# Optimization experiments

Hardware: AMD Instinct MI355X
Metric: run time of the kernel (lower is better)

The kernel has to match this reference:

```python
import jax, jax.numpy as jnp
import numpy as np

E = 8          # num_global_experts
K = 2          # top-k
D = 1024       # model_dim
H = 4096       # hidden_size_per_expert
CAP_FACTOR = 1.0


def setup_inputs() -> dict:
    key = jax.random.key(0)
    ks = jax.random.split(key, 5)
    x = jax.random.normal(ks[0], (4, 2048, D), jnp.float32)
    gate_w = jax.random.normal(ks[1], (E, D), jnp.float32) * 0.02
    fc1_w = jax.random.normal(ks[2], (E, H, D), jnp.float32) * 0.02
    fc1_b = jnp.zeros((E, 1, H), jnp.float32)
    fc2_w = jax.random.normal(ks[3], (E, H, D), jnp.float32) * 0.02
    fc2_b = jnp.zeros((E, 1, D), jnp.float32)
    return {"x": x, "gate_w": gate_w, "fc1_w": fc1_w, "fc1_b": fc1_b,
            "fc2_w": fc2_w, "fc2_b": fc2_b}


def reference(x, gate_w, fc1_w, fc1_b, fc2_w, fc2_b):
    B, S, Dm = x.shape
    xf = x.reshape(-1, Dm)                       # [N, D] tokens
    N = xf.shape[0]
    cap = int(K * CAP_FACTOR * ((N + E - 1) // E))  # expert capacity

    # ---- gating (top-k softmax, normalized) ----
    logits = xf @ gate_w.T                       # [N, E]
    scores = jax.nn.softmax(logits, axis=-1)
    topv, topi = jax.lax.top_k(scores, K)        # [N, K]
    gates = topv / jnp.sum(topv, axis=-1, keepdims=True)

    # ---- per-slot locations within each expert (sequential over K slots) ----
    offset = jnp.zeros((E,), jnp.int32)
    locs = []
    for j in range(K):
        mask = jax.nn.one_hot(topi[:, j], E, dtype=jnp.int32)   # [N, E]
        loc_in = jnp.cumsum(mask, axis=0) - 1 + offset[None, :]
        locs.append(jnp.take_along_axis(loc_in, topi[:, j:j + 1], axis=1)[:, 0])
        offset = offset + mask.sum(axis=0)
    loc = jnp.stack(locs, axis=1)                # [N, K]
    valid = loc < cap                            # capacity-dropped tokens
    flat_idx = jnp.where(valid, topi * cap + loc, 0)   # [N, K]
    w = valid.astype(xf.dtype)

    # ---- dispatch (scatter tokens into [E, cap, D], postscore => unweighted) ----
    disp = jnp.zeros((E * cap, Dm), xf.dtype)
    disp = disp.at[flat_idx.reshape(-1)].add(
        (xf[:, None, :] * w[:, :, None]).reshape(-1, Dm))
    de = disp.reshape(E, cap, Dm)

    # ---- batched expert FFN: relu(x @ fc1^T + b1) @ fc2 + b2 ----
    h = jax.nn.relu(jnp.einsum('ecd,ehd->ech', de, fc1_w) + fc1_b)
    eo = jnp.einsum('ech,ehd->ecd', h, fc2_w) + fc2_b

    # ---- combine (gather + gate-weighted sum over K slots) ----
    gathered = eo.reshape(E * cap, Dm)[flat_idx]       # [N, K, D]
    out = jnp.sum(gathered * (gates * w)[:, :, None], axis=1)
    return out.reshape(B, S, Dm)
```

## Files before the change

### kernel.cpp

```cpp
#include <hip/hip_runtime.h>
#include <hip/hip_bf16.h>
#include <stdint.h>

#define NEXP 8
#define DM   1024
#define HID  4096
#define NTOK 8192
#define CAPS 2048

#define BM 256
#define BN 256
#define BK 64

typedef __attribute__((ext_vector_type(8))) short bh8_t;
typedef __attribute__((ext_vector_type(4))) float f32x4_t;
typedef unsigned short u16;

static __device__ __forceinline__ u16 f2bf(float f) {
    __hip_bfloat16 h = __float2bfloat16(f);
    return __builtin_bit_cast(u16, h);
}
static __device__ __forceinline__ float bf2f(u16 u) {
    unsigned int x = ((unsigned int)u) << 16;
    return __builtin_bit_cast(float, x);
}

#define FENCE asm volatile("" ::: "memory")
#define BAR   do { FENCE; __builtin_amdgcn_s_barrier(); FENCE; } while (0)
#define LGKM0 do { asm volatile("s_waitcnt lgkmcnt(0)" ::: "memory"); \
                   __builtin_amdgcn_sched_barrier(0); } while (0)
#define MFMA(d, a, b) d = __builtin_amdgcn_mfma_f32_16x16x32_bf16(a, b, d, 0, 0, 0)

__global__ __launch_bounds__(256) void k_conv_bf16(const float* __restrict__ in,
                                                   u16* __restrict__ out, long n) {
    long i = ((long)blockIdx.x * 256 + threadIdx.x) * 4;
    if (i >= n) return;
    float4 v = *(const float4*)(in + i);
    ushort4 o;
    o.x = f2bf(v.x); o.y = f2bf(v.y); o.z = f2bf(v.z); o.w = f2bf(v.w);
    *(ushort4*)(out + i) = o;
}

__global__ __launch_bounds__(256) void k_transpose_w2(const float* __restrict__ in,
                                                      u16* __restrict__ out) {
    int e = blockIdx.z;
    const float* I = in + (long)e * HID * DM;
    u16* O = out + (long)e * DM * HID;
    __shared__ float t[32][33];
    int x = threadIdx.x & 31, y = threadIdx.x >> 5;
    int h0 = blockIdx.x * 32, d0 = blockIdx.y * 32;
    #pragma unroll
    for (int i = 0; i < 4; ++i)
        t[y + 8*i][x] = I[(long)(h0 + y + 8*i) * DM + d0 + x];
    __syncthreads();
    #pragma unroll
    for (int i = 0; i < 4; ++i)
        O[(long)(d0 + y + 8*i) * HID + h0 + x] = f2bf(t[x][y + 8*i]);
}

__global__ __launch_bounds__(256) void k_gating(const float* __restrict__ x,
        const float* __restrict__ gw, int* __restrict__ topi, float* __restrict__ gates) {
    __shared__ float sg[NEXP][DM];
    int tid = threadIdx.x;
    for (int i = tid; i < NEXP*DM; i += 256) ((float*)sg)[i] = gw[i];
    __syncthreads();
    int lane = tid & 63, w = tid >> 6;
    long n = (long)blockIdx.x * 4 + w;
    const float* xr = x + n * DM;
    float acc[NEXP] = {};
    for (int i = 0; i < DM/64; ++i) {
        float xv = xr[lane + i*64];
        #pragma unroll
        for (int e = 0; e < NEXP; ++e) acc[e] += xv * sg[e][lane + i*64];
    }
    #pragma unroll
    for (int e = 0; e < NEXP; ++e)
        #pragma unroll
        for (int off = 32; off; off >>= 1) acc[e] += __shfl_xor(acc[e], off);
    if (lane == 0) {
        float mx = acc[0];
        #pragma unroll
        for (int e = 1; e < NEXP; ++e) mx = fmaxf(mx, acc[e]);
        float p[NEXP];
        #pragma unroll
        for (int e = 0; e < NEXP; ++e) p[e] = expf(acc[e] - mx);
        float v0 = p[0]; int i0 = 0;
        #pragma unroll
        for (int e = 1; e < NEXP; ++e) if (p[e] > v0) { v0 = p[e]; i0 = e; }
        float v1 = -1.f; int i1 = 0;
        #pragma unroll
        for (int e = 0; e < NEXP; ++e) if (e != i0 && p[e] > v1) { v1 = p[e]; i1 = e; }
        float tot = v0 + v1;
        topi[n*2]   = i0; topi[n*2+1] = i1;
        gates[n*2]  = v0 / tot; gates[n*2+1] = v1 / tot;
    }
}

__global__ __launch_bounds__(64) void k_locate(const int* __restrict__ topi,
                                               int* __restrict__ flat) {
    int lane = threadIdx.x;
    const int TPL = NTOK / 64;
    int base = lane * TPL;
    int offset[NEXP];
    #pragma unroll
    for (int e = 0; e < NEXP; ++e) offset[e] = 0;
    for (int j = 0; j < 2; ++j) {
        unsigned long long pk = 0;
        for (int t = 0; t < TPL; ++t) {
            int e = topi[(long)(base + t)*2 + j];
            pk += 1ull << (8*e);
        }
        int cnt[NEXP], excl[NEXP];
        #pragma unroll
        for (int e = 0; e < NEXP; ++e) cnt[e] = (int)((pk >> (8*e)) & 0xff);
        #pragma unroll
        for (int e = 0; e < NEXP; ++e) {
            int v = cnt[e];
            for (int d = 1; d < 64; d <<= 1) {
                int o = __shfl_up(v, d);
                if (lane >= d) v += o;
            }
            excl[e] = v - cnt[e] + offset[e];
            offset[e] += __shfl(v, 63);
        }
        unsigned long long lo = 0, hi = 0;
        #pragma unroll
        for (int e = 0; e < 4; ++e)    lo |= (unsigned long long)(excl[e] & 0xffff) << (16*e);
        #pragma unroll
        for (int e = 4; e < NEXP; ++e) hi |= (unsigned long long)(excl[e] & 0xffff) << (16*(e-4));
        for (int t = 0; t < TPL; ++t) {
            long n = base + t;
            int e = topi[n*2 + j];
            int sh = 16 * (e & 3);
            int loc;
            if (e < 4) { loc = (int)((lo >> sh) & 0xffff); lo += 1ull << sh; }
            else       { loc = (int)((hi >> sh) & 0xffff); hi += 1ull << sh; }
            flat[n*2 + j] = (loc < CAPS) ? (e * CAPS + loc) : -1;
        }
    }
}

__global__ __launch_bounds__(256) void k_dispatch(const float* __restrict__ x,
        const int* __restrict__ flat, u16* __restrict__ disp) {
    long n = blockIdx.x;
    int tid = threadIdx.x;
    float4 v = *(const float4*)(x + n*DM + tid*4);
    ushort4 o; o.x = f2bf(v.x); o.y = f2bf(v.y); o.z = f2bf(v.z); o.w = f2bf(v.w);
    int f0 = flat[n*2], f1 = flat[n*2+1];
    if (f0 >= 0) *(ushort4*)(disp + (long)f0*DM + tid*4) = o;
    if (f1 >= 0) *(ushort4*)(disp + (long)f1*DM + tid*4) = o;
}

static __device__ __forceinline__ void stage_half(const u16* __restrict__ g, int ld,
                                                  u16* R, int wid, int lane) {
    int rlo = wid*8 + (lane >> 3);
    int cbe = ((lane & 7) ^ ((lane >> 3) & 7)) * 8;
    const u16* s0 = g + (long)rlo * ld + cbe;
    const u16* s1 = g + (long)(rlo + 64) * ld + cbe;
    u16* d0 = R + wid*512 + lane*8;
    u16* d1 = R + 4096 + wid*512 + lane*8;
    __builtin_amdgcn_global_load_lds((const __attribute__((address_space(1))) void*)s0,
        (__attribute__((address_space(3))) void*)d0, 16, 0, 0);
    __builtin_amdgcn_global_load_lds((const __attribute__((address_space(1))) void*)s1,
        (__attribute__((address_space(3))) void*)d1, 16, 0, 0);
}

template<int RELU>
__global__ __launch_bounds__(512, 2)
void k_gemm8(const u16* __restrict__ A, const u16* __restrict__ B,
             const float* __restrict__ bias, u16* __restrict__ C,
             int N, int K, long strA, long strB, long strBias, long strC)
{
    __shared__ u16 sm[2][2][2][8192];

    int gx = gridDim.x, gy = gridDim.y;
    int nwg = gx * gy * (int)gridDim.z;
    int lin = blockIdx.x + gx * (blockIdx.y + gy * blockIdx.z);
    int qq  = nwg >> 3;
    int swz = (lin & 7) * qq + (lin >> 3);
    int gxy = gx * gy;
    int bz = swz / gxy, rm = swz % gxy, by = rm / gx, bx = rm % gx;

    const u16* Ae = A + (long)bz * strA;
    const u16* Be = B + (long)bz * strB;
    const float* bi = bias + (long)bz * strBias;
    u16* Ce = C + (long)bz * strC;

    long tm = (long)by * BM, tn = (long)bx * BN;
    const u16* Abase = Ae + tm * (long)K;
    const u16* Bbase = Be + tn * (long)K;

    int tid = threadIdx.x, lane = tid & 63, wid = tid >> 6;
    int wr = wid >> 2, wc = wid & 3;

    int frow = lane & 15;
    int fc0 = (((lane >> 4) * 16)      ^ ((lane & 7) << 4)) >> 1;
    int fc1 = ((64 + (lane >> 4) * 16) ^ ((lane & 7) << 4)) >> 1;

    const int NT = K / BK;

    f32x4_t acc[8][4] = {};

    auto STG = [&](int buf, int ab, int half, int kt) {
        const u16* g = (ab ? Bbase : Abase) + (long)(half * 128) * K + (long)kt * BK;
        stage_half(g, K, &sm[buf][ab][half][0], wid, lane);
    };
    auto LDA = [&](int c, int mi, int kk) -> bh8_t {
        const u16* p = &sm[c][0][wr][0] + (mi * 16 + frow) * 64 + (kk ? fc1 : fc0);
        return *(const bh8_t*)p;
    };
    auto LDB = [&](int c, int ni, int kk) -> bh8_t {
        const u16* p = &sm[c][1][wc >> 1][0] + ((wc & 1) * 64 + ni * 16 + frow) * 64 + (kk ? fc1 : fc0);
        return *(const bh8_t*)p;
    };

    auto ktile = [&](int c, int kt, int s12, int s34, int vm) {
        bh8_t a0[4][2], a1[4][2], bf[4][2];
        #pragma unroll
        for (int mi = 0; mi < 4; ++mi) { a0[mi][0] = LDA(c, mi, 0); a0[mi][1] = LDA(c, mi, 1); }
        #pragma unroll
        for (int ni = 0; ni < 2; ++ni) { bf[ni][0] = LDB(c, ni, 0); bf[ni][1] = LDB(c, ni, 1); }
        if (s12) STG(c ^ 1, 0, 1, kt + 1);
        BAR; LGKM0;
        __builtin_amdgcn_s_setprio(1);
        #pragma unroll
        for (int mi = 0; mi < 4; ++mi)
            #pragma unroll
            for (int ni = 0; ni < 2; ++ni)
                #pragma unroll
                for (int kk = 0; kk < 2; ++kk) MFMA(acc[mi][ni], a0[mi][kk], bf[ni][kk]);
        __builtin_amdgcn_s_setprio(0);
        __builtin_amdgcn_sched_barrier(0);
        BAR;
        #pragma unroll
        for (int ni = 2; ni < 4; ++ni) { bf[ni][0] = LDB(c, ni, 0); bf[ni][1] = LDB(c, ni, 1); }
        if (s12) STG(c ^ 1, 1, 1, kt + 1);
        BAR; LGKM0;
        __builtin_amdgcn_s_setprio(1);
        #pragma unroll
        for (int mi = 0; mi < 4; ++mi)
            #pragma unroll
            for (int ni = 2; ni < 4; ++ni)
                #pragma unroll
                for (int kk = 0; kk < 2; ++kk) MFMA(acc[mi][ni], a0[mi][kk], bf[ni][kk]);
        __builtin_amdgcn_s_setprio(0);
        __builtin_amdgcn_sched_barrier(0);
        BAR;
        #pragma unroll
        for (int mi = 0; mi < 4; ++mi) { a1[mi][0] = LDA(c, mi + 4, 0); a1[mi][1] = LDA(c, mi + 4, 1); }
        if (s34) STG(c, 1, 0, kt + 2);
        BAR; LGKM0;
        __builtin_amdgcn_s_setprio(1);
        #pragma unroll
        for (int mi = 0; mi < 4; ++mi)
            #pragma unroll
            for (int ni = 0; ni < 2; ++ni)
                #pragma unroll
                for (int kk = 0; kk < 2; ++kk) MFMA(acc[mi + 4][ni], a1[mi][kk], bf[ni][kk]);
        __builtin_amdgcn_s_setprio(0);
        __builtin_amdgcn_sched_barrier(0);
        BAR;
        if (s34) STG(c, 0, 0, kt + 2);
        if (vm == 4)      { asm volatile("s_waitcnt vmcnt(4)" ::: "memory"); }
        else if (vm == 0) { asm volatile("s_waitcnt vmcnt(0)" ::: "memory"); }
        BAR; LGKM0;
        __builtin_amdgcn_s_setprio(1);
        #pragma unroll
        for (int mi = 0; mi < 4; ++mi)
            #pragma unroll
            for (int ni = 2; ni < 4; ++ni)
                #pragma unroll
                for (int kk = 0; kk < 2; ++kk) MFMA(acc[mi + 4][ni], a1[mi][kk], bf[ni][kk]);
        __builtin_amdgcn_s_setprio(0);
        __builtin_amdgcn_sched_barrier(0);
        BAR;
    };

    STG(0, 0, 0, 0); STG(0, 0, 1, 0); STG(0, 1, 0, 0); STG(0, 1, 1, 0);
    STG(1, 1, 0, 1); STG(1, 0, 0, 1);
    asm volatile("s_waitcnt vmcnt(4)" ::: "memory");
    BAR;

    int kt = 0;
    for (; kt < NT - 2; ++kt) ktile(kt & 1, kt, 1, 1, 4);
    ktile(kt & 1, kt, 1, 0, 0); ++kt;
    ktile(kt & 1, kt, 0, 0, -1);

    u16* wb = &sm[0][0][0][0] + wid * 8192;
    #pragma unroll
    for (int mi = 0; mi < 8; ++mi)
        #pragma unroll
        for (int ni = 0; ni < 4; ++ni) {
            float bv = bi[tn + wc * 64 + ni * 16 + (lane & 15)];
            #pragma unroll
            for (int r = 0; r < 4; ++r) {
                int row = mi * 16 + (lane >> 4) * 4 + r;
                int ce  = ni * 16 + (lane & 15);
                float v = acc[mi][ni][r] + bv;
                if (RELU) v = fmaxf(v, 0.f);
                wb[row * 64 + (ce ^ ((row & 7) << 3))] = f2bf(v);
            }
        }
    __syncthreads();
    long crow = tm + wr * 128;
    long ccol = tn + wc * 64 + (lane & 7) * 8;
    #pragma unroll
    for (int i = 0; i < 16; ++i) {
        int rr = i * 8 + (lane >> 3);
        bh8_t v = *(const bh8_t*)(wb + rr * 64 + (((lane & 7) * 8) ^ ((rr & 7) << 3)));
        *(bh8_t*)(Ce + (crow + rr) * N + ccol) = v;
    }
}

__global__ __launch_bounds__(256) void k_combine(const u16* __restrict__ eo,
        const int* __restrict__ flat, const float* __restrict__ gates,
        float* __restrict__ out) {
    long n = blockIdx.x;
    int tid = threadIdx.x;
    int f0 = flat[n*2], f1 = flat[n*2+1];
    float g0 = (f0 >= 0) ? gates[n*2]   : 0.f;
    float g1 = (f1 >= 0) ? gates[n*2+1] : 0.f;
    const u16* r0 = eo + (long)(f0 >= 0 ? f0 : 0) * DM;
    const u16* r1 = eo + (long)(f1 >= 0 ? f1 : 0) * DM;
    ushort4 a = *(const ushort4*)(r0 + tid*4);
    ushort4 b = *(const ushort4*)(r1 + tid*4);
    float4 o;
    o.x = g0*bf2f(a.x) + g1*bf2f(b.x);
    o.y = g0*bf2f(a.y) + g1*bf2f(b.y);
    o.z = g0*bf2f(a.z) + g1*bf2f(b.z);
    o.w = g0*bf2f(a.w) + g1*bf2f(b.w);
    *(float4*)(out + n*DM + tid*4) = o;
}

extern "C" void kernel_launch(void* const* d_in, const int* in_sizes, int n_in,
                              void* d_out, int out_size, void* d_ws, size_t ws_size,
                              hipStream_t stream) {
    const float* x    = (const float*)d_in[0];
    const float* gw   = (const float*)d_in[1];
    const float* fc1w = (const float*)d_in[2];
    const float* fc1b = (const float*)d_in[3];
    const float* fc2w = (const float*)d_in[4];
    const float* fc2b = (const float*)d_in[5];
    float* out = (float*)d_out;
    char* ws = (char*)d_ws;

    u16* disp = (u16*)(ws);
    u16* eo   = disp;
    u16* h    = (u16*)(ws + 33554432L);
    u16* w1b  = (u16*)(ws + 33554432L + 134217728L);
    u16* w2t  = (u16*)(ws + 33554432L + 134217728L + 67108864L);
    char* tail = ws + 33554432L + 134217728L + 67108864L + 67108864L;
    int*   topi  = (int*)tail;
    float* gates = (float*)(tail + 65536);
    int*   flat  = (int*)(tail + 131072);

    long n1 = (long)NEXP * HID * DM;

    hipMemsetAsync(disp, 0, (size_t)NEXP * CAPS * DM * 2, stream);
    k_conv_bf16<<<dim3(n1/1024), 256, 0, stream>>>(fc1w, w1b, n1);
    k_transpose_w2<<<dim3(HID/32, DM/32, NEXP), 256, 0, stream>>>(fc2w, w2t);
    k_gating<<<dim3(NTOK/4), 256, 0, stream>>>(x, gw, topi, gates);
    k_locate<<<dim3(1), 64, 0, stream>>>(topi, flat);
    k_dispatch<<<dim3(NTOK), 256, 0, stream>>>(x, flat, disp);
    k_gemm8<1><<<dim3(HID/BN, CAPS/BM, NEXP), 512, 0, stream>>>(
        disp, w1b, fc1b, h, HID, DM,
        (long)CAPS*DM, (long)HID*DM, (long)HID, (long)CAPS*HID);
    k_gemm8<0><<<dim3(DM/BN, CAPS/BM, NEXP), 512, 0, stream>>>(
        h, w2t, fc2b, eo, DM, HID,
        (long)CAPS*HID, (long)DM*HID, (long)DM, (long)CAPS*DM);
    k_combine<<<dim3(NTOK), 256, 0, stream>>>(eo, flat, gates, out);
}
```

Before: 471.9 us.

## Drop dispatch memset, vectorize W2 transpose, parallelize locate, relax GEMM LDS waits

Removes the zero-fill of the dispatch buffer. Unfilled capacity rows are computed independently and never gathered by combine, so the result does not depend on them. The fc2 transpose moves to 64x64 tiles with float4 loads and 16-byte bf16 stores. The single-wave locate kernel becomes a 256-thread block that stages topi in LDS and combines per-wave scans through shared sums. The GEMM also drops the explicit lgkmcnt(0) waits before each MFMA group and leaves LDS dependency waits to the compiler, which cuts stalls but adds scheduling risk.

```diff
diff --git a/kernel.cpp b/kernel.cpp
--- a/kernel.cpp
+++ b/kernel.cpp
@@ -27,8 +27,7 @@
 
 #define FENCE asm volatile("" ::: "memory")
 #define BAR   do { FENCE; __builtin_amdgcn_s_barrier(); FENCE; } while (0)
-#define LGKM0 do { asm volatile("s_waitcnt lgkmcnt(0)" ::: "memory"); \
-                   __builtin_amdgcn_sched_barrier(0); } while (0)
+#define SB0   __builtin_amdgcn_sched_barrier(0)
 #define MFMA(d, a, b) d = __builtin_amdgcn_mfma_f32_16x16x32_bf16(a, b, d, 0, 0, 0)
 
 __global__ __launch_bounds__(256) void k_conv_bf16(const float* __restrict__ in,
@@ -46,16 +45,28 @@
     int e = blockIdx.z;
     const float* I = in + (long)e * HID * DM;
     u16* O = out + (long)e * DM * HID;
-    __shared__ float t[32][33];
-    int x = threadIdx.x & 31, y = threadIdx.x >> 5;
-    int h0 = blockIdx.x * 32, d0 = blockIdx.y * 32;
-    #pragma unroll
-    for (int i = 0; i < 4; ++i)
-        t[y + 8*i][x] = I[(long)(h0 + y + 8*i) * DM + d0 + x];
+    __shared__ float t[64][65];
+    int h0 = blockIdx.x * 64, d0 = blockIdx.y * 64;
+    int tid = threadIdx.x;
+    int r = tid >> 4, cw = (tid & 15) * 4;
+    #pragma unroll
+    for (int i = 0; i < 4; ++i) {
+        float4 v = *(const float4*)(I + (long)(h0 + r + 16*i) * DM + d0 + cw);
+        t[r + 16*i][cw]     = v.x;
+        t[r + 16*i][cw + 1] = v.y;
+        t[r + 16*i][cw + 2] = v.z;
+        t[r + 16*i][cw + 3] = v.w;
+    }
     __syncthreads();
-    #pragma unroll
-    for (int i = 0; i < 4; ++i)
-        O[(long)(d0 + y + 8*i) * HID + h0 + x] = f2bf(t[x][y + 8*i]);
+    int dl = tid >> 2, hc = (tid & 3) * 16;
+    bh8_t w0, w1;
+    #pragma unroll
+    for (int j = 0; j < 8; ++j) w0[j] = (short)f2bf(t[hc + j][dl]);
+    #pragma unroll
+    for (int j = 0; j < 8; ++j) w1[j] = (short)f2bf(t[hc + 8 + j][dl]);
+    u16* o = O + (long)(d0 + dl) * HID + h0 + hc;
+    *(bh8_t*)o = w0;
+    *(bh8_t*)(o + 8) = w1;
 }
 
 __global__ __launch_bounds__(256) void k_gating(const float* __restrict__ x,
@@ -96,32 +107,42 @@
     }
 }
 
-__global__ __launch_bounds__(64) void k_locate(const int* __restrict__ topi,
-                                               int* __restrict__ flat) {
-    int lane = threadIdx.x;
-    const int TPL = NTOK / 64;
-    int base = lane * TPL;
+__global__ __launch_bounds__(256) void k_locate(const int* __restrict__ topi,
+                                                int* __restrict__ flat) {
+    __shared__ int st[NTOK * 2];
+    __shared__ int wsum[4];
+    int tid = threadIdx.x, lane = tid & 63, w = tid >> 6;
+    int4* st4 = (int4*)st;
+    const int4* g4 = (const int4*)topi;
+    for (int i = tid; i < NTOK * 2 / 4; i += 256) st4[i] = g4[i];
+    __syncthreads();
+    const int TPL = NTOK / 256;
+    int base = tid * TPL;
     int offset[NEXP];
     #pragma unroll
     for (int e = 0; e < NEXP; ++e) offset[e] = 0;
     for (int j = 0; j < 2; ++j) {
         unsigned long long pk = 0;
-        for (int t = 0; t < TPL; ++t) {
-            int e = topi[(long)(base + t)*2 + j];
-            pk += 1ull << (8*e);
-        }
-        int cnt[NEXP], excl[NEXP];
-        #pragma unroll
-        for (int e = 0; e < NEXP; ++e) cnt[e] = (int)((pk >> (8*e)) & 0xff);
+        for (int t = 0; t < TPL; ++t) pk += 1ull << (8 * st[(base + t) * 2 + j]);
+        int excl[NEXP];
         #pragma unroll
         for (int e = 0; e < NEXP; ++e) {
-            int v = cnt[e];
+            int cnt = (int)((pk >> (8 * e)) & 0xff);
+            int v = cnt;
+            #pragma unroll
             for (int d = 1; d < 64; d <<= 1) {
                 int o = __shfl_up(v, d);
                 if (lane >= d) v += o;
             }
-            excl[e] = v - cnt[e] + offset[e];
-            offset[e] += __shfl(v, 63);
+            if (lane == 63) wsum[w] = v;
+            __syncthreads();
+            int wb = 0;
+            #pragma unroll
+            for (int ww = 0; ww < 4; ++ww) if (ww < w) wb += wsum[ww];
+            int tot = wsum[0] + wsum[1] + wsum[2] + wsum[3];
+            excl[e] = v - cnt + wb + offset[e];
+            offset[e] += tot;
+            __syncthreads();
         }
         unsigned long long lo = 0, hi = 0;
         #pragma unroll
@@ -129,15 +150,18 @@
         #pragma unroll
         for (int e = 4; e < NEXP; ++e) hi |= (unsigned long long)(excl[e] & 0xffff) << (16*(e-4));
         for (int t = 0; t < TPL; ++t) {
-            long n = base + t;
-            int e = topi[n*2 + j];
+            int n = base + t;
+            int e = st[n * 2 + j];
             int sh = 16 * (e & 3);
             int loc;
             if (e < 4) { loc = (int)((lo >> sh) & 0xffff); lo += 1ull << sh; }
             else       { loc = (int)((hi >> sh) & 0xffff); hi += 1ull << sh; }
-            flat[n*2 + j] = (loc < CAPS) ? (e * CAPS + loc) : -1;
+            st[n * 2 + j] = (loc < CAPS) ? (e * CAPS + loc) : -1;
         }
-    }
+        __syncthreads();
+    }
+    int4* f4 = (int4*)flat;
+    for (int i = tid; i < NTOK * 2 / 4; i += 256) f4[i] = st4[i];
 }
 
 __global__ __launch_bounds__(256) void k_dispatch(const float* __restrict__ x,
@@ -182,13 +206,12 @@
     int bz = swz / gxy, rm = swz % gxy, by = rm / gx, bx = rm % gx;
 
     const u16* Ae = A + (long)bz * strA;
-    const u16* Be = B + (long)bz * strB;
     const float* bi = bias + (long)bz * strBias;
     u16* Ce = C + (long)bz * strC;
 
     long tm = (long)by * BM, tn = (long)bx * BN;
     const u16* Abase = Ae + tm * (long)K;
-    const u16* Bbase = Be + tn * (long)K;
+    const u16* Bbase = B + (long)bz * strB + tn * (long)K;
 
     int tid = threadIdx.x, lane = tid & 63, wid = tid >> 6;
     int wr = wid >> 2, wc = wid & 3;
@@ -221,7 +244,7 @@
         #pragma unroll
         for (int ni = 0; ni < 2; ++ni) { bf[ni][0] = LDB(c, ni, 0); bf[ni][1] = LDB(c, ni, 1); }
         if (s12) STG(c ^ 1, 0, 1, kt + 1);
-        BAR; LGKM0;
+        BAR;
         __builtin_amdgcn_s_setprio(1);
         #pragma unroll
         for (int mi = 0; mi < 4; ++mi)
@@ -229,13 +252,11 @@
             for (int ni = 0; ni < 2; ++ni)
                 #pragma unroll
                 for (int kk = 0; kk < 2; ++kk) MFMA(acc[mi][ni], a0[mi][kk], bf[ni][kk]);
-        __builtin_amdgcn_s_setprio(0);
-        __builtin_amdgcn_sched_barrier(0);
-        BAR;
+        __builtin_amdgcn_s_setprio(0); SB0; BAR;
         #pragma unroll
         for (int ni = 2; ni < 4; ++ni) { bf[ni][0] = LDB(c, ni, 0); bf[ni][1] = LDB(c, ni, 1); }
         if (s12) STG(c ^ 1, 1, 1, kt + 1);
-        BAR; LGKM0;
+        BAR;
         __builtin_amdgcn_s_setprio(1);
         #pragma unroll
         for (int mi = 0; mi < 4; ++mi)
@@ -243,13 +264,11 @@
             for (int ni = 2; ni < 4; ++ni)
                 #pragma unroll
                 for (int kk = 0; kk < 2; ++kk) MFMA(acc[mi][ni], a0[mi][kk], bf[ni][kk]);
-        __builtin_amdgcn_s_setprio(0);
-        __builtin_amdgcn_sched_barrier(0);
-        BAR;
+        __builtin_amdgcn_s_setprio(0); SB0; BAR;
         #pragma unroll
         for (int mi = 0; mi < 4; ++mi) { a1[mi][0] = LDA(c, mi + 4, 0); a1[mi][1] = LDA(c, mi + 4, 1); }
         if (s34) STG(c, 1, 0, kt + 2);
-        BAR; LGKM0;
+        BAR;
         __builtin_amdgcn_s_setprio(1);
         #pragma unroll
         for (int mi = 0; mi < 4; ++mi)
@@ -257,13 +276,11 @@
             for (int ni = 0; ni < 2; ++ni)
                 #pragma unroll
                 for (int kk = 0; kk < 2; ++kk) MFMA(acc[mi + 4][ni], a1[mi][kk], bf[ni][kk]);
-        __builtin_amdgcn_s_setprio(0);
-        __builtin_amdgcn_sched_barrier(0);
-        BAR;
+        __builtin_amdgcn_s_setprio(0); SB0; BAR;
         if (s34) STG(c, 0, 0, kt + 2);
         if (vm == 4)      { asm volatile("s_waitcnt vmcnt(4)" ::: "memory"); }
         else if (vm == 0) { asm volatile("s_waitcnt vmcnt(0)" ::: "memory"); }
-        BAR; LGKM0;
+        BAR;
         __builtin_amdgcn_s_setprio(1);
         #pragma unroll
         for (int mi = 0; mi < 4; ++mi)
@@ -271,9 +288,7 @@
             for (int ni = 2; ni < 4; ++ni)
                 #pragma unroll
                 for (int kk = 0; kk < 2; ++kk) MFMA(acc[mi + 4][ni], a1[mi][kk], bf[ni][kk]);
-        __builtin_amdgcn_s_setprio(0);
-        __builtin_amdgcn_sched_barrier(0);
-        BAR;
+        __builtin_amdgcn_s_setprio(0); SB0; BAR;
     };
 
     STG(0, 0, 0, 0); STG(0, 0, 1, 0); STG(0, 1, 0, 0); STG(0, 1, 1, 0);
@@ -356,11 +371,10 @@
 
     long n1 = (long)NEXP * HID * DM;
 
-    hipMemsetAsync(disp, 0, (size_t)NEXP * CAPS * DM * 2, stream);
     k_conv_bf16<<<dim3(n1/1024), 256, 0, stream>>>(fc1w, w1b, n1);
-    k_transpose_w2<<<dim3(HID/32, DM/32, NEXP), 256, 0, stream>>>(fc2w, w2t);
+    k_transpose_w2<<<dim3(HID/64, DM/64, NEXP), 256, 0, stream>>>(fc2w, w2t);
     k_gating<<<dim3(NTOK/4), 256, 0, stream>>>(x, gw, topi, gates);
-    k_locate<<<dim3(1), 64, 0, stream>>>(topi, flat);
+    k_locate<<<dim3(1), 256, 0, stream>>>(topi, flat);
     k_dispatch<<<dim3(NTOK), 256, 0, stream>>>(x, flat, disp);
     k_gemm8<1><<<dim3(HID/BN, CAPS/BM, NEXP), 512, 0, stream>>>(
         disp, w1b, fc1b, h, HID, DM,
```

New measurement: 398.8 us. 1.18x faster.
